# Kernel optimization log

Measured on AMD Instinct MI355X. Metric: run time of the kernel, lower is better.

The kernel has to match this reference:

```python
import jax, jax.numpy as jnp
import numpy as np

B, T, SEG = 64, 16, 50          # batch, n segments, segment length (cap 50 in original)
E, D, H, F = 512, 512, 8, 2048  # dim_embeddings, dim_encoder, n_heads, dim_ff
DH = D // H
SCALE = float(1.0 / np.sqrt(DH))


def _ln(x, g, b):
    m = jnp.mean(x, -1, keepdims=True)
    v = jnp.var(x, -1, keepdims=True)
    return (x - m) * jax.lax.rsqrt(v + 1e-5) * g + b


def _mha(q_in, kv_in, Wq, Wk, Wv, Wo, kv_lens):
    b, sq, _ = q_in.shape
    sk = kv_in.shape[1]
    q = (q_in @ Wq).reshape(b, sq, H, DH)
    k = (kv_in @ Wk).reshape(b, sk, H, DH)
    v = (kv_in @ Wv).reshape(b, sk, H, DH)
    scores = jnp.einsum('bqhd,bkhd->bhqk', q, k) * SCALE
    mask = jnp.arange(sk)[None, :] < kv_lens[:, None]  # [b, sk] key-padding mask
    scores = jnp.where(mask[:, None, None, :], scores, -1e9)
    a = jax.nn.softmax(scores, axis=-1)
    o = jnp.einsum('bhqk,bkhd->bqhd', a, v).reshape(b, sq, D)
    return o @ Wo


def _ffn(x, W1, W2):
    return jax.nn.relu(x @ W1) @ W2


def _encoder(x, lens, p):
    # TransformerEncoder: project E->D, masked self-attn + FFN, post-LN residuals
    h = x @ p['eWin']
    h = _ln(h + _mha(h, h, p['eWq'], p['eWk'], p['eWv'], p['eWo'], lens), p['eG1'], p['eB1'])
    return _ln(h + _ffn(h, p['eF1'], p['eF2']), p['eG2'], p['eB2'])


def _connection(prev, curr, prev_lens, p):
    # Connection: curr cross-attends over prev (masked by prev_lens) + FFN
    h = _ln(curr + _mha(curr, prev, p['cWq'], p['cWk'], p['cWv'], p['cWo'], prev_lens), p['cG1'], p['cB1'])
    return _ln(h + _ffn(h, p['cF1'], p['cF2']), p['cG2'], p['cB2'])


def _forward(seqs, ends, p):
    first_lens = jnp.minimum(ends[:, 0], SEG)
    encoded = _encoder(seqs[:, :SEG], first_lens, p)  # [B, SEG, D]
    # regular segmentation: ends[b,t] = (t+1)*SEG, so every step uses a full segment
    segs = seqs.reshape(B, T, SEG, E).transpose(1, 0, 2, 3)[1:]        # [T-1, B, SEG, E]
    seg_lens = jnp.minimum(ends[:, 1:] - ends[:, :-1], SEG).T          # [T-1, B]
    prev_lens = jnp.full((B,), SEG, jnp.int32)

    def step(enc, xs):
        seg, lens = xs
        currs = _encoder(seg, lens, p)
        out = _connection(enc, currs, prev_lens, p)
        return out, None  # out[-SEG:] == out since seq_len = min(diff, 50) = SEG

    encoded, _ = jax.lax.scan(step, encoded, (segs, seg_lens))
    return encoded


def setup_inputs():
    key = jax.random.key(0)
    ks = jax.random.split(key, 16)
    g = lambda k, s: jax.random.normal(k, s, jnp.float32) * 0.02
    inp = {
        'seqs': jax.random.normal(ks[0], (B, T * SEG, E), jnp.float32),
        'ends': jnp.broadcast_to((jnp.arange(1, T + 1) * SEG).astype(jnp.int32), (B, T)),
        'eWin': g(ks[1], (E, D)),
        'eWq': g(ks[2], (D, D)), 'eWk': g(ks[3], (D, D)),
        'eWv': g(ks[4], (D, D)), 'eWo': g(ks[5], (D, D)),
        'eG1': jnp.ones(D), 'eB1': jnp.zeros(D),
        'eF1': g(ks[6], (D, F)), 'eF2': g(ks[7], (F, D)),
        'eG2': jnp.ones(D), 'eB2': jnp.zeros(D),
        'cWq': g(ks[8], (D, D)), 'cWk': g(ks[9], (D, D)),
        'cWv': g(ks[10], (D, D)), 'cWo': g(ks[11], (D, D)),
        'cG1': jnp.ones(D), 'cB1': jnp.zeros(D),
        'cF1': g(ks[12], (D, F)), 'cF2': g(ks[13], (F, D)),
        'cG2': jnp.ones(D), 'cB2': jnp.zeros(D),
    }
    return inp


def reference(seqs, ends, eWin, eWq, eWk, eWv, eWo, eG1, eB1, eF1, eF2, eG2, eB2,
              cWq, cWk, cWv, cWo, cG1, cB1, cF1, cF2, cG2, cB2):
    p = dict(eWin=eWin, eWq=eWq, eWk=eWk, eWv=eWv, eWo=eWo, eG1=eG1, eB1=eB1,
             eF1=eF1, eF2=eF2, eG2=eG2, eB2=eB2, cWq=cWq, cWk=cWk, cWv=cWv,
             cWo=cWo, cG1=cG1, cB1=cB1, cF1=cF1, cF2=cF2, cG2=cG2, cB2=cB2)
    return _forward(seqs, ends, p)
```

## Files before the change

kernel.cpp:

```cpp
#include <hip/hip_runtime.h>


#define NB   64
#define NT   16
#define SEGL 50
#define DMODEL 512
#define DFF  2048
#define NHEAD 8
#define DHEAD 64

typedef unsigned short ushort_t;
typedef __attribute__((ext_vector_type(8))) short bfrag;
typedef __attribute__((ext_vector_type(4))) float ffrag;

__device__ __forceinline__ ushort_t f2b(float x) {
    union { float f; unsigned u; } c; c.f = x;
    unsigned r = c.u + 0x7fffu + ((c.u >> 16) & 1u);
    return (ushort_t)(r >> 16);
}

#define GLOAD_LDS16(g, l) __builtin_amdgcn_global_load_lds( \
    (const __attribute__((address_space(1))) void*)(g),      \
    (__attribute__((address_space(3))) void*)(l), 16, 0, 0)

template<int BM, int BN, int WROWS, int WCOLS>
__global__ __launch_bounds__(256) void mfma_gemm(
    const ushort_t* __restrict__ A, int agrp, long long astride,
    const ushort_t* __restrict__ Bt, ushort_t* __restrict__ C,
    int M, int N, int K, int relu)
{
    constexpr int WM = BM / WROWS, WN = BN / WCOLS;
    constexpr int SM = WM / 16, SN = WN / 16;
    constexpr int NSUBA = BM / 16, NSUBB = BN / 16;
    constexpr int NSUB = NSUBA + NSUBB;
    constexpr int NINST = NSUB * 2;
    constexpr int IPW = NINST / 4;
    constexpr int BUFS = NSUB * 1024;
    constexpr int EST = WN + 8;
    constexpr int LDS_KLOOP = 2 * BUFS;
    constexpr int LDS_EPI   = 4 * WM * EST;
    constexpr int LDS_SZ = LDS_KLOOP > LDS_EPI ? LDS_KLOOP : LDS_EPI;
    __shared__ ushort_t lds[LDS_SZ];

    const int tid = threadIdx.x;
    const int wave = tid >> 6, lane = tid & 63;
    const int wrow = wave / WCOLS, wcol = wave % WCOLS;
    const int bm = blockIdx.y * BM, bn = blockIdx.x * BN;
    const int lm = lane & 15, lq = lane >> 4;

    ffrag acc[SM][SN];
#pragma unroll
    for (int i = 0; i < SM; ++i)
#pragma unroll
        for (int j = 0; j < SN; ++j) acc[i][j] = (ffrag){0.f, 0.f, 0.f, 0.f};

    const ushort_t* gptr[IPW];
    int loff[IPW];
#pragma unroll
    for (int e = 0; e < IPW; ++e) {
        int g = wave * IPW + e;
        int s = g >> 1, h = g & 1;
        if (s < NSUBA) {
            int m = bm + s * 16 + lm;
            gptr[e] = A + (long long)(m / agrp) * astride
                        + (long long)(m % agrp) * K + h * 32 + lq * 8;
        } else {
            int n = bn + (s - NSUBA) * 16 + lm;
            gptr[e] = Bt + (long long)n * K + h * 32 + lq * 8;
        }
        loff[e] = s * 1024 + h * 512;
    }

#pragma unroll
    for (int e = 0; e < IPW; ++e)
        GLOAD_LDS16(gptr[e], &lds[loff[e]]);

    const int nk = K >> 6;
    for (int kk = 0; kk < nk; ++kk) {
        __syncthreads();
        if (kk + 1 < nk) {
            const int koff = (kk + 1) << 6;
            const int nb = (kk + 1) & 1;
#pragma unroll
            for (int e = 0; e < IPW; ++e)
                GLOAD_LDS16(gptr[e] + koff, &lds[nb * BUFS + loff[e]]);
        }
        const ushort_t* lb = &lds[(kk & 1) * BUFS];
#pragma unroll
        for (int h = 0; h < 2; ++h) {
            bfrag af[SM], bfg[SN];
#pragma unroll
            for (int i = 0; i < SM; ++i)
                af[i] = *(const bfrag*)&lb[(wrow * SM + i) * 1024 + h * 512 + lane * 8];
#pragma unroll
            for (int j = 0; j < SN; ++j)
                bfg[j] = *(const bfrag*)&lb[(NSUBA + wcol * SN + j) * 1024 + h * 512 + lane * 8];
#pragma unroll
            for (int i = 0; i < SM; ++i)
#pragma unroll
                for (int j = 0; j < SN; ++j)
                    acc[i][j] = __builtin_amdgcn_mfma_f32_16x16x32_bf16(
                        af[i], bfg[j], acc[i][j], 0, 0, 0);
        }
    }

    __syncthreads();
    ushort_t* ep = &lds[wave * WM * EST];
#pragma unroll
    for (int i = 0; i < SM; ++i)
#pragma unroll
        for (int j = 0; j < SN; ++j)
#pragma unroll
            for (int r = 0; r < 4; ++r) {
                int row = i * 16 + lq * 4 + r;
                int col = j * 16 + lm;
                float v = acc[i][j][r];
                if (relu) v = fmaxf(v, 0.f);
                ep[row * EST + col] = f2b(v);
            }
    constexpr int CPR = WN / 8;
    constexpr int RPI = 64 / CPR;
    const int lrow = lane / CPR, lcol = (lane % CPR) * 8;
#pragma unroll
    for (int it = 0; it < WM / RPI; ++it) {
        int row = it * RPI + lrow;
        uint4 v = *(const uint4*)&ep[row * EST + lcol];
        long long grow = bm + wrow * WM + row;
        int gcol = bn + wcol * WN + lcol;
        *(uint4*)&C[grow * N + gcol] = v;
    }
}

__global__ __launch_bounds__(256) void wtrans_k(
    const float* __restrict__ W, ushort_t* __restrict__ Wt, int K, int N)
{
    __shared__ float t[32][33];
    const int bk = blockIdx.y * 32, bn = blockIdx.x * 32;
    const int tx = threadIdx.x & 31, ty = threadIdx.x >> 5;
    for (int i = ty; i < 32; i += 8)
        t[i][tx] = W[(long long)(bk + i) * N + bn + tx];
    __syncthreads();
    for (int i = ty; i < 32; i += 8)
        Wt[(long long)(bn + i) * K + bk + tx] = f2b(t[tx][i]);
}

__global__ __launch_bounds__(256) void cvt_k(
    const float* __restrict__ in, ushort_t* __restrict__ out, long long n)
{
    long long i = ((long long)blockIdx.x * 256 + threadIdx.x) * 8;
    if (i >= n) return;
    float4 a = *(const float4*)(in + i);
    float4 b = *(const float4*)(in + i + 4);
    ushort_t o[8] = {f2b(a.x), f2b(a.y), f2b(a.z), f2b(a.w),
                     f2b(b.x), f2b(b.y), f2b(b.z), f2b(b.w)};
    *(uint4*)(out + i) = *(const uint4*)o;
}

__global__ __launch_bounds__(256) void attn_mfma_k(
    const ushort_t* __restrict__ Q, long long qns, long long qrs,
    const ushort_t* __restrict__ K, const ushort_t* __restrict__ V,
    long long kns, long long kvrs,
    ushort_t* __restrict__ O,
    const int* __restrict__ lens, int G, int t0)
{
    __shared__ ushort_t qs[64][72];
    __shared__ ushort_t ks[64][72];
    __shared__ ushort_t vt[64][72];
    const int n = blockIdx.x >> 3, h = blockIdx.x & 7;
    const int tid = threadIdx.x;
    const int wave = tid >> 6, lane = tid & 63;
    const int lm = lane & 15, lq = lane >> 4;
    int len = SEGL;
    if (lens) {
        int b = n / G, t = t0 + (n % G);
        len = lens[b * NT + t];
        if (len > SEGL) len = SEGL;
    }
    {
        uint4 z = {0, 0, 0, 0};
        uint4* vz = (uint4*)&vt[0][0];
        for (int i = tid; i < 64 * 72 / 8; i += 256) vz[i] = z;
    }
    __syncthreads();
    for (int idx = tid; idx < SEGL * 8; idx += 256) {
        int s = idx >> 3, d8 = (idx & 7) << 3;
        const ushort_t* qp = Q + (long long)n * qns + (long long)s * qrs + h * DHEAD + d8;
        const ushort_t* kp = K + (long long)n * kns + (long long)s * kvrs + h * DHEAD + d8;
        const ushort_t* vp = V + (long long)n * kns + (long long)s * kvrs + h * DHEAD + d8;
        *(uint4*)&qs[s][d8] = *(const uint4*)qp;
        *(uint4*)&ks[s][d8] = *(const uint4*)kp;
        uint4 v4 = *(const uint4*)vp;
        const ushort_t* vv = (const ushort_t*)&v4;
#pragma unroll
        for (int u = 0; u < 8; ++u) vt[d8 + u][s] = vv[u];
    }
    __syncthreads();

    ffrag sc[4];
#pragma unroll
    for (int nt = 0; nt < 4; ++nt) sc[nt] = (ffrag){0.f, 0.f, 0.f, 0.f};
#pragma unroll
    for (int kt = 0; kt < 2; ++kt) {
        bfrag a = *(const bfrag*)&qs[wave * 16 + lm][kt * 32 + lq * 8];
#pragma unroll
        for (int nt = 0; nt < 4; ++nt) {
            bfrag b = *(const bfrag*)&ks[nt * 16 + lm][kt * 32 + lq * 8];
            sc[nt] = __builtin_amdgcn_mfma_f32_16x16x32_bf16(a, b, sc[nt], 0, 0, 0);
        }
    }
    __syncthreads();

#pragma unroll
    for (int r = 0; r < 4; ++r) {
        float x[4];
        float mx = -1e30f;
#pragma unroll
        for (int nt = 0; nt < 4; ++nt) {
            int col = nt * 16 + lm;
            x[nt] = (col < len) ? sc[nt][r] * 0.125f : -1e9f;
            mx = fmaxf(mx, x[nt]);
        }
        for (int off = 8; off; off >>= 1) mx = fmaxf(mx, __shfl_xor(mx, off));
        float e[4], se = 0.f;
#pragma unroll
        for (int nt = 0; nt < 4; ++nt) { e[nt] = __expf(x[nt] - mx); se += e[nt]; }
        for (int off = 8; off; off >>= 1) se += __shfl_xor(se, off);
        float inv = 1.f / se;
        int row = wave * 16 + lq * 4 + r;
#pragma unroll
        for (int nt = 0; nt < 4; ++nt)
            qs[row][nt * 16 + lm] = f2b(e[nt] * inv);
    }
    __syncthreads();

    ffrag oc[4];
#pragma unroll
    for (int dt = 0; dt < 4; ++dt) oc[dt] = (ffrag){0.f, 0.f, 0.f, 0.f};
#pragma unroll
    for (int kt = 0; kt < 2; ++kt) {
        bfrag a = *(const bfrag*)&qs[wave * 16 + lm][kt * 32 + lq * 8];
#pragma unroll
        for (int dt = 0; dt < 4; ++dt) {
            bfrag b = *(const bfrag*)&vt[dt * 16 + lm][kt * 32 + lq * 8];
            oc[dt] = __builtin_amdgcn_mfma_f32_16x16x32_bf16(a, b, oc[dt], 0, 0, 0);
        }
    }
#pragma unroll
    for (int r = 0; r < 4; ++r) {
        int i = wave * 16 + lq * 4 + r;
        if (i < SEGL) {
            ushort_t* op = O + (long long)(n * SEGL + i) * DMODEL + h * DHEAD + lm;
#pragma unroll
            for (int dt = 0; dt < 4; ++dt)
                op[dt * 16] = f2b(oc[dt][r]);
        }
    }
}

__global__ __launch_bounds__(256) void cross_attn_k(
    const ushort_t* __restrict__ Qp, long long qns, long long qrs,
    const ushort_t* __restrict__ Prev, int pgrp, long long pstride,
    const ushort_t* __restrict__ Wkv,
    ushort_t* __restrict__ O)
{
    __shared__ ushort_t xp[64 * 264];
    __shared__ ushort_t qs[64][72];
    const int n = blockIdx.x >> 3, h = blockIdx.x & 7;
    const int tid = threadIdx.x;
    const int wave = tid >> 6, lane = tid & 63;
    const int lm = lane & 15, lq = lane >> 4;

    for (int idx = tid; idx < SEGL * 8; idx += 256) {
        int s = idx >> 3, d8 = (idx & 7) << 3;
        *(uint4*)&qs[s][d8] =
            *(const uint4*)(Qp + (long long)n * qns + (long long)s * qrs + h * DHEAD + d8);
    }

    const ushort_t* wbase = Wkv +
        (long long)((wave >> 1) * 512 + h * 64 + (wave & 1) * 32) * 512;
    ffrag kv[4][2];
#pragma unroll
    for (int i = 0; i < 4; ++i)
#pragma unroll
        for (int j = 0; j < 2; ++j) kv[i][j] = (ffrag){0.f, 0.f, 0.f, 0.f};

#pragma unroll
    for (int half = 0; half < 2; ++half) {
        __syncthreads();
        for (int idx = tid; idx < 64 * 33; idx += 256) {
            int s = idx / 33, c8 = (idx % 33) * 8;
            uint4 v = {0, 0, 0, 0};
            if (s < SEGL && c8 < 256) {
                long long r = (long long)n * SEGL + s;
                v = *(const uint4*)(Prev + (r / pgrp) * pstride
                                    + (r % pgrp) * DMODEL + half * 256 + c8);
            }
            *(uint4*)&xp[s * 264 + c8] = v;
        }
        __syncthreads();
#pragma unroll
        for (int k8 = 0; k8 < 8; ++k8) {
            const int kg = half * 256 + k8 * 32;
            bfrag bf[2], af[4];
#pragma unroll
            for (int j = 0; j < 2; ++j)
                bf[j] = *(const bfrag*)(wbase + (long long)(j * 16 + lm) * 512 + kg + lq * 8);
#pragma unroll
            for (int i = 0; i < 4; ++i)
                af[i] = *(const bfrag*)&xp[(i * 16 + lm) * 264 + k8 * 32 + lq * 8];
#pragma unroll
            for (int i = 0; i < 4; ++i)
#pragma unroll
                for (int j = 0; j < 2; ++j)
                    kv[i][j] = __builtin_amdgcn_mfma_f32_16x16x32_bf16(
                        af[i], bf[j], kv[i][j], 0, 0, 0);
        }
    }
    __syncthreads();
    ushort_t (*ks)[72] = (ushort_t(*)[72])&xp[0];
    ushort_t (*vt)[72] = (ushort_t(*)[72])&xp[64 * 72];
#pragma unroll
    for (int i = 0; i < 4; ++i)
#pragma unroll
        for (int j = 0; j < 2; ++j)
#pragma unroll
            for (int r = 0; r < 4; ++r) {
                int rowk = i * 16 + lq * 4 + r;
                int d = (wave & 1) * 32 + j * 16 + lm;
                ushort_t val = f2b(kv[i][j][r]);
                if (wave < 2) ks[rowk][d] = val;
                else          vt[d][rowk] = val;
            }
    __syncthreads();

    ffrag sc[4];
#pragma unroll
    for (int nt = 0; nt < 4; ++nt) sc[nt] = (ffrag){0.f, 0.f, 0.f, 0.f};
#pragma unroll
    for (int kt = 0; kt < 2; ++kt) {
        bfrag a = *(const bfrag*)&qs[wave * 16 + lm][kt * 32 + lq * 8];
#pragma unroll
        for (int nt = 0; nt < 4; ++nt) {
            bfrag b = *(const bfrag*)&ks[nt * 16 + lm][kt * 32 + lq * 8];
            sc[nt] = __builtin_amdgcn_mfma_f32_16x16x32_bf16(a, b, sc[nt], 0, 0, 0);
        }
    }
    __syncthreads();

#pragma unroll
    for (int r = 0; r < 4; ++r) {
        float x[4];
        float mx = -1e30f;
#pragma unroll
        for (int nt = 0; nt < 4; ++nt) {
            int col = nt * 16 + lm;
            x[nt] = (col < SEGL) ? sc[nt][r] * 0.125f : -1e9f;
            mx = fmaxf(mx, x[nt]);
        }
        for (int off = 8; off; off >>= 1) mx = fmaxf(mx, __shfl_xor(mx, off));
        float e[4], se = 0.f;
#pragma unroll
        for (int nt = 0; nt < 4; ++nt) { e[nt] = __expf(x[nt] - mx); se += e[nt]; }
        for (int off = 8; off; off >>= 1) se += __shfl_xor(se, off);
        float inv = 1.f / se;
        int row = wave * 16 + lq * 4 + r;
#pragma unroll
        for (int nt = 0; nt < 4; ++nt)
            qs[row][nt * 16 + lm] = f2b(e[nt] * inv);
    }
    __syncthreads();

    ffrag oc[4];
#pragma unroll
    for (int dt = 0; dt < 4; ++dt) oc[dt] = (ffrag){0.f, 0.f, 0.f, 0.f};
#pragma unroll
    for (int kt = 0; kt < 2; ++kt) {
        bfrag a = *(const bfrag*)&qs[wave * 16 + lm][kt * 32 + lq * 8];
#pragma unroll
        for (int dt = 0; dt < 4; ++dt) {
            bfrag b = *(const bfrag*)&vt[dt * 16 + lm][kt * 32 + lq * 8];
            oc[dt] = __builtin_amdgcn_mfma_f32_16x16x32_bf16(a, b, oc[dt], 0, 0, 0);
        }
    }
#pragma unroll
    for (int r = 0; r < 4; ++r) {
        int i = wave * 16 + lq * 4 + r;
        if (i < SEGL) {
            ushort_t* op = O + (long long)(n * SEGL + i) * DMODEL + h * DHEAD + lm;
#pragma unroll
            for (int dt = 0; dt < 4; ++dt)
                op[dt * 16] = f2b(oc[dt][r]);
        }
    }
}

template<bool OUTF32>
__global__ __launch_bounds__(256) void add_ln_k(
    const ushort_t* __restrict__ A, int agrp, long long astride,
    const ushort_t* __restrict__ Bv,
    const float* __restrict__ gamma, const float* __restrict__ beta,
    void* __restrict__ O, int ogrp, long long ostride, int M)
{
    const int wave = threadIdx.x >> 6, lane = threadIdx.x & 63;
    const int r = blockIdx.x * 4 + wave;
    if (r >= M) return;
    const ushort_t* a = A + (long long)(r / agrp) * astride + (long long)(r % agrp) * DMODEL;
    const ushort_t* b = Bv + (long long)r * DMODEL;
    float x[8];
    {
        uint4 a4 = *(const uint4*)(a + lane * 8);
        uint4 b4 = *(const uint4*)(b + lane * 8);
        const unsigned* aa = (const unsigned*)&a4;
        const unsigned* bb = (const unsigned*)&b4;
#pragma unroll
        for (int c = 0; c < 4; ++c) {
            union { unsigned u; float f; } alo, ahi, blo, bhi;
            alo.u = aa[c] << 16; ahi.u = aa[c] & 0xffff0000u;
            blo.u = bb[c] << 16; bhi.u = bb[c] & 0xffff0000u;
            x[2 * c]     = alo.f + blo.f;
            x[2 * c + 1] = ahi.f + bhi.f;
        }
    }
    float s = 0.f, s2 = 0.f;
#pragma unroll
    for (int i = 0; i < 8; ++i) { s += x[i]; s2 = fmaf(x[i], x[i], s2); }
    for (int off = 32; off; off >>= 1) {
        s += __shfl_xor(s, off);
        s2 += __shfl_xor(s2, off);
    }
    const float mean = s * (1.f / DMODEL);
    const float var = s2 * (1.f / DMODEL) - mean * mean;
    const float inv = rsqrtf(var + 1e-5f);
    float4 g0 = *(const float4*)(gamma + lane * 8);
    float4 g1 = *(const float4*)(gamma + lane * 8 + 4);
    float4 be0 = *(const float4*)(beta + lane * 8);
    float4 be1 = *(const float4*)(beta + lane * 8 + 4);
    float y[8];
    y[0] = (x[0] - mean) * inv * g0.x + be0.x;
    y[1] = (x[1] - mean) * inv * g0.y + be0.y;
    y[2] = (x[2] - mean) * inv * g0.z + be0.z;
    y[3] = (x[3] - mean) * inv * g0.w + be0.w;
    y[4] = (x[4] - mean) * inv * g1.x + be1.x;
    y[5] = (x[5] - mean) * inv * g1.y + be1.y;
    y[6] = (x[6] - mean) * inv * g1.z + be1.z;
    y[7] = (x[7] - mean) * inv * g1.w + be1.w;
    if (OUTF32) {
        float* o = (float*)O + (long long)(r / ogrp) * ostride + (long long)(r % ogrp) * DMODEL;
        *(float4*)(o + lane * 8) = *(float4*)&y[0];
        *(float4*)(o + lane * 8 + 4) = *(float4*)&y[4];
    } else {
        ushort_t* o = (ushort_t*)O + (long long)(r / ogrp) * ostride + (long long)(r % ogrp) * DMODEL;
        ushort_t ob[8];
#pragma unroll
        for (int i = 0; i < 8; ++i) ob[i] = f2b(y[i]);
        *(uint4*)(o + lane * 8) = *(const uint4*)ob;
    }
}

__global__ void lens_k(const int* __restrict__ ends, int* __restrict__ lens)
{
    int i = blockIdx.x * 256 + threadIdx.x;
    if (i >= NB * NT) return;
    int t = i & (NT - 1);
    int prev = t ? ends[i - 1] : 0;
    int l = ends[i] - prev;
    if (l > SEGL) l = SEGL;
    lens[i] = l;
}

extern "C" void kernel_launch(void* const* d_in, const int* in_sizes, int n_in,
                              void* d_out, int out_size, void* d_ws, size_t ws_size,
                              hipStream_t stream)
{
    const float* seqs = (const float*)d_in[0];
    const int*   ends = (const int*)d_in[1];
    const float* eG1 = (const float*)d_in[7],  *eB1 = (const float*)d_in[8];
    const float* eG2 = (const float*)d_in[11], *eB2 = (const float*)d_in[12];
    const float* cG1 = (const float*)d_in[17], *cB1 = (const float*)d_in[18];
    const float* cG2 = (const float*)d_in[21], *cB2 = (const float*)d_in[22];
    float* out = (float*)d_out;

    const int G = (ws_size >= (size_t)470000000) ? 8 : 4;
    const long long CH = 1638400LL * G;

    ushort_t* ws = (ushort_t*)d_ws;
    const long long SEQROW = (long long)NT * SEGL * DMODEL;
    ushort_t* SEQB = ws;
    ushort_t* WT   = SEQB + 26214400LL;
    ushort_t* ENC  = WT   + 6553600LL;
    ushort_t* BUF0 = ENC  + 26214400LL;
    ushort_t* QKV  = BUF0 + CH;
    ushort_t* BUF4 = QKV  + 3 * CH;
    ushort_t* BUF1 = BUF4 + CH;
    ushort_t* BUF2 = BUF1 + CH;
    ushort_t* MID  = BUF2 + CH;
    ushort_t* OUTB = MID  + 4 * CH;
    ushort_t* QALL = OUTB + 1638400LL;
    int*      lens = (int*)(QALL + 24576000LL);

    const ushort_t* eWinT = WT + 0;
    const ushort_t* WQKVe = WT + 262144;
    const ushort_t* eWoT  = WT + 1048576;
    const ushort_t* eF1T  = WT + 1310720;
    const ushort_t* eF2T  = WT + 2359296;
    const ushort_t* cWqT  = WT + 3407872;
    const ushort_t* cKV   = WT + 3670016;
    const ushort_t* cWoT  = WT + 4194304;
    const ushort_t* cF1T  = WT + 4456448;
    const ushort_t* cF2T  = WT + 5505024;

    struct WMap { int src; long long dst; int K, N; };
    const WMap wm[13] = {
        {2,  0,       512, 512},
        {3,  262144,  512, 512},
        {4,  524288,  512, 512},
        {5,  786432,  512, 512},
        {6,  1048576, 512, 512},
        {9,  1310720, 512, 2048},
        {10, 2359296, 2048, 512},
        {13, 3407872, 512, 512},
        {14, 3670016, 512, 512},
        {15, 3932160, 512, 512},
        {16, 4194304, 512, 512},
        {19, 4456448, 512, 2048},
        {20, 5505024, 2048, 512},
    };

    cvt_k<<<12800, 256, 0, stream>>>(seqs, SEQB, 26214400LL);
    for (int w = 0; w < 13; ++w) {
        dim3 g(wm[w].N / 32, wm[w].K / 32);
        wtrans_k<<<g, 256, 0, stream>>>((const float*)d_in[wm[w].src],
                                        WT + wm[w].dst, wm[w].K, wm[w].N);
    }
    lens_k<<<4, 256, 0, stream>>>(ends, lens);

    auto gemmL = [&](const ushort_t* A, int agrp, long long astr, const ushort_t* Bt,
                     ushort_t* C, int M, int N, int K, int relu) {
        dim3 g(N / 128, M / 128);
        mfma_gemm<128, 128, 2, 2><<<g, 256, 0, stream>>>(A, agrp, astr, Bt, C, M, N, K, relu);
    };
    auto gemmS = [&](const ushort_t* A, int agrp, long long astr, const ushort_t* Bt,
                     ushort_t* C, int M, int N, int K, int relu) {
        dim3 g(N / 64, M / 64);
        mfma_gemm<64, 64, 2, 2><<<g, 256, 0, stream>>>(A, agrp, astr, Bt, C, M, N, K, relu);
    };

    const int Mc = NB * G * SEGL;
    for (int c = 0; c < NT / G; ++c) {
        const int t0 = c * G;
        const ushort_t* Abase = SEQB + (long long)t0 * SEGL * DMODEL;
        ushort_t* ENCc = ENC + (long long)t0 * SEGL * DMODEL;
        gemmL(Abase, G * SEGL, SEQROW, eWinT, BUF0, Mc, 512, 512, 0);
        gemmL(BUF0, Mc, 0, WQKVe, QKV, Mc, 1536, 512, 0);
        attn_mfma_k<<<NB * G * NHEAD, 256, 0, stream>>>(
            QKV, 50LL * 1536, 1536, QKV + 512, QKV + 1024, 50LL * 1536, 1536,
            BUF4, lens, G, t0);
        gemmL(BUF4, Mc, 0, eWoT, BUF1, Mc, 512, 512, 0);
        add_ln_k<false><<<Mc / 4, 256, 0, stream>>>(BUF0, Mc, 0, BUF1, eG1, eB1,
                                                    BUF2, Mc, 0, Mc);
        gemmL(BUF2, Mc, 0, eF1T, MID, Mc, 2048, 512, 1);
        gemmL(MID, Mc, 0, eF2T, BUF1, Mc, 512, 2048, 0);
        add_ln_k<false><<<Mc / 4, 256, 0, stream>>>(BUF2, Mc, 0, BUF1, eG2, eB2,
                                                    ENCc, G * SEGL, SEQROW, Mc);
    }

    gemmL(ENC + 25600, 750, SEQROW, cWqT, QALL, 48000, 512, 512, 0);

    const int Ms = NB * SEGL;
    for (int t = 1; t < NT; ++t) {
        const ushort_t* currA = ENC + (long long)t * SEGL * DMODEL;
        const ushort_t* prevA; int pg; long long ps;
        if (t == 1) { prevA = ENC;  pg = SEGL; ps = SEQROW; }
        else        { prevA = OUTB; pg = Ms;   ps = 0; }
        cross_attn_k<<<NB * NHEAD, 256, 0, stream>>>(
            QALL + (long long)(t - 1) * 25600, 750LL * 512, 512,
            prevA, pg, ps, cKV, BUF4);
        gemmS(BUF4, Ms, 0, cWoT, BUF0, Ms, 512, 512, 0);
        add_ln_k<false><<<Ms / 4, 256, 0, stream>>>(currA, SEGL, SEQROW, BUF0, cG1, cB1,
                                                    BUF2, Ms, 0, Ms);
        gemmS(BUF2, Ms, 0, cF1T, MID, Ms, 2048, 512, 1);
        gemmS(MID, Ms, 0, cF2T, BUF0, Ms, 512, 2048, 0);
        if (t == NT - 1)
            add_ln_k<true><<<Ms / 4, 256, 0, stream>>>(BUF2, Ms, 0, BUF0, cG2, cB2,
                                                       out, Ms, 0, Ms);
        else
            add_ln_k<false><<<Ms / 4, 256, 0, stream>>>(BUF2, Ms, 0, BUF0, cG2, cB2,
                                                        OUTB, Ms, 0, Ms);
    }
}
```

Measured before the change: 2.770 ms.

## Fuse sequential connection-stage loop into one persistent kernel with grid barriers

Replaces the 15-step host loop of six launches per step (cross-attention, Wo GEMM, add+LN, two FFN GEMMs, add+LN) with one persistent kernel. Work items are grid-strided and the phases are separated by an atomic-counter grid barrier that lens_k resets. The goal is to remove about 90 kernel launches and their inter-kernel gaps on the serial critical path. The risks are barrier spin cost, a deadlock-avoidance timeout that could silently break correctness, and the assumption that every block is co-resident (grid of 256 or 512 chosen from occupancy).

```diff
diff --git a/kernel.cpp b/kernel.cpp
--- a/kernel.cpp
+++ b/kernel.cpp
@@ -218,143 +218,6 @@
         for (int nt = 0; nt < 4; ++nt) {
             int col = nt * 16 + lm;
             x[nt] = (col < len) ? sc[nt][r] * 0.125f : -1e9f;
-            mx = fmaxf(mx, x[nt]);
-        }
-        for (int off = 8; off; off >>= 1) mx = fmaxf(mx, __shfl_xor(mx, off));
-        float e[4], se = 0.f;
-#pragma unroll
-        for (int nt = 0; nt < 4; ++nt) { e[nt] = __expf(x[nt] - mx); se += e[nt]; }
-        for (int off = 8; off; off >>= 1) se += __shfl_xor(se, off);
-        float inv = 1.f / se;
-        int row = wave * 16 + lq * 4 + r;
-#pragma unroll
-        for (int nt = 0; nt < 4; ++nt)
-            qs[row][nt * 16 + lm] = f2b(e[nt] * inv);
-    }
-    __syncthreads();
-
-    ffrag oc[4];
-#pragma unroll
-    for (int dt = 0; dt < 4; ++dt) oc[dt] = (ffrag){0.f, 0.f, 0.f, 0.f};
-#pragma unroll
-    for (int kt = 0; kt < 2; ++kt) {
-        bfrag a = *(const bfrag*)&qs[wave * 16 + lm][kt * 32 + lq * 8];
-#pragma unroll
-        for (int dt = 0; dt < 4; ++dt) {
-            bfrag b = *(const bfrag*)&vt[dt * 16 + lm][kt * 32 + lq * 8];
-            oc[dt] = __builtin_amdgcn_mfma_f32_16x16x32_bf16(a, b, oc[dt], 0, 0, 0);
-        }
-    }
-#pragma unroll
-    for (int r = 0; r < 4; ++r) {
-        int i = wave * 16 + lq * 4 + r;
-        if (i < SEGL) {
-            ushort_t* op = O + (long long)(n * SEGL + i) * DMODEL + h * DHEAD + lm;
-#pragma unroll
-            for (int dt = 0; dt < 4; ++dt)
-                op[dt * 16] = f2b(oc[dt][r]);
-        }
-    }
-}
-
-__global__ __launch_bounds__(256) void cross_attn_k(
-    const ushort_t* __restrict__ Qp, long long qns, long long qrs,
-    const ushort_t* __restrict__ Prev, int pgrp, long long pstride,
-    const ushort_t* __restrict__ Wkv,
-    ushort_t* __restrict__ O)
-{
-    __shared__ ushort_t xp[64 * 264];
-    __shared__ ushort_t qs[64][72];
-    const int n = blockIdx.x >> 3, h = blockIdx.x & 7;
-    const int tid = threadIdx.x;
-    const int wave = tid >> 6, lane = tid & 63;
-    const int lm = lane & 15, lq = lane >> 4;
-
-    for (int idx = tid; idx < SEGL * 8; idx += 256) {
-        int s = idx >> 3, d8 = (idx & 7) << 3;
-        *(uint4*)&qs[s][d8] =
-            *(const uint4*)(Qp + (long long)n * qns + (long long)s * qrs + h * DHEAD + d8);
-    }
-
-    const ushort_t* wbase = Wkv +
-        (long long)((wave >> 1) * 512 + h * 64 + (wave & 1) * 32) * 512;
-    ffrag kv[4][2];
-#pragma unroll
-    for (int i = 0; i < 4; ++i)
-#pragma unroll
-        for (int j = 0; j < 2; ++j) kv[i][j] = (ffrag){0.f, 0.f, 0.f, 0.f};
-
-#pragma unroll
-    for (int half = 0; half < 2; ++half) {
-        __syncthreads();
-        for (int idx = tid; idx < 64 * 33; idx += 256) {
-            int s = idx / 33, c8 = (idx % 33) * 8;
-            uint4 v = {0, 0, 0, 0};
-            if (s < SEGL && c8 < 256) {
-                long long r = (long long)n * SEGL + s;
-                v = *(const uint4*)(Prev + (r / pgrp) * pstride
-                                    + (r % pgrp) * DMODEL + half * 256 + c8);
-            }
-            *(uint4*)&xp[s * 264 + c8] = v;
-        }
-        __syncthreads();
-#pragma unroll
-        for (int k8 = 0; k8 < 8; ++k8) {
-            const int kg = half * 256 + k8 * 32;
-            bfrag bf[2], af[4];
-#pragma unroll
-            for (int j = 0; j < 2; ++j)
-                bf[j] = *(const bfrag*)(wbase + (long long)(j * 16 + lm) * 512 + kg + lq * 8);
-#pragma unroll
-            for (int i = 0; i < 4; ++i)
-                af[i] = *(const bfrag*)&xp[(i * 16 + lm) * 264 + k8 * 32 + lq * 8];
-#pragma unroll
-            for (int i = 0; i < 4; ++i)
-#pragma unroll
-                for (int j = 0; j < 2; ++j)
-                    kv[i][j] = __builtin_amdgcn_mfma_f32_16x16x32_bf16(
-                        af[i], bf[j], kv[i][j], 0, 0, 0);
-        }
-    }
-    __syncthreads();
-    ushort_t (*ks)[72] = (ushort_t(*)[72])&xp[0];
-    ushort_t (*vt)[72] = (ushort_t(*)[72])&xp[64 * 72];
-#pragma unroll
-    for (int i = 0; i < 4; ++i)
-#pragma unroll
-        for (int j = 0; j < 2; ++j)
-#pragma unroll
-            for (int r = 0; r < 4; ++r) {
-                int rowk = i * 16 + lq * 4 + r;
-                int d = (wave & 1) * 32 + j * 16 + lm;
-                ushort_t val = f2b(kv[i][j][r]);
-                if (wave < 2) ks[rowk][d] = val;
-                else          vt[d][rowk] = val;
-            }
-    __syncthreads();
-
-    ffrag sc[4];
-#pragma unroll
-    for (int nt = 0; nt < 4; ++nt) sc[nt] = (ffrag){0.f, 0.f, 0.f, 0.f};
-#pragma unroll
-    for (int kt = 0; kt < 2; ++kt) {
-        bfrag a = *(const bfrag*)&qs[wave * 16 + lm][kt * 32 + lq * 8];
-#pragma unroll
-        for (int nt = 0; nt < 4; ++nt) {
-            bfrag b = *(const bfrag*)&ks[nt * 16 + lm][kt * 32 + lq * 8];
-            sc[nt] = __builtin_amdgcn_mfma_f32_16x16x32_bf16(a, b, sc[nt], 0, 0, 0);
-        }
-    }
-    __syncthreads();
-
-#pragma unroll
-    for (int r = 0; r < 4; ++r) {
-        float x[4];
-        float mx = -1e30f;
-#pragma unroll
-        for (int nt = 0; nt < 4; ++nt) {
-            int col = nt * 16 + lm;
-            x[nt] = (col < SEGL) ? sc[nt][r] * 0.125f : -1e9f;
             mx = fmaxf(mx, x[nt]);
         }
         for (int off = 8; off; off >>= 1) mx = fmaxf(mx, __shfl_xor(mx, off));
@@ -457,15 +320,389 @@
     }
 }
 
-__global__ void lens_k(const int* __restrict__ ends, int* __restrict__ lens)
+__global__ void lens_k(const int* __restrict__ ends, int* __restrict__ lens,
+                       unsigned* __restrict__ bar)
 {
     int i = blockIdx.x * 256 + threadIdx.x;
+    if (blockIdx.x == 0 && threadIdx.x == 0) *bar = 0;
     if (i >= NB * NT) return;
     int t = i & (NT - 1);
     int prev = t ? ends[i - 1] : 0;
     int l = ends[i] - prev;
     if (l > SEGL) l = SEGL;
     lens[i] = l;
+}
+
+
+__device__ __forceinline__ void gbar(unsigned* bar, unsigned target)
+{
+    __syncthreads();
+    if (threadIdx.x == 0) {
+        __threadfence();
+        __hip_atomic_fetch_add(bar, 1u, __ATOMIC_RELAXED, __HIP_MEMORY_SCOPE_AGENT);
+        int spins = 0;
+        while (__hip_atomic_load(bar, __ATOMIC_RELAXED, __HIP_MEMORY_SCOPE_AGENT) < target) {
+            __builtin_amdgcn_s_sleep(8);
+            if (++spins > (1 << 20)) break;
+        }
+        __threadfence();
+    }
+    __syncthreads();
+}
+
+__device__ void dev_gemm64(ushort_t* lds, int u,
+    const ushort_t* __restrict__ A, int agrp, long long astride,
+    const ushort_t* __restrict__ Bt, ushort_t* __restrict__ C,
+    int M, int N, int K, int relu)
+{
+    const int tid = threadIdx.x;
+    const int wave = tid >> 6, lane = tid & 63;
+    const int wrow = wave >> 1, wcol = wave & 1;
+    const int nbx = N >> 6;
+    const int bm = (u / nbx) << 6, bn = (u % nbx) << 6;
+    const int lm = lane & 15, lq = lane >> 4;
+
+    __syncthreads();
+
+    ffrag acc[2][2];
+#pragma unroll
+    for (int i = 0; i < 2; ++i)
+#pragma unroll
+        for (int j = 0; j < 2; ++j) acc[i][j] = (ffrag){0.f, 0.f, 0.f, 0.f};
+
+    const ushort_t* gptr[4];
+    int loff[4];
+#pragma unroll
+    for (int e = 0; e < 4; ++e) {
+        int g = wave * 4 + e;
+        int s = g >> 1, h = g & 1;
+        if (s < 4) {
+            int m = bm + s * 16 + lm;
+            gptr[e] = A + (long long)(m / agrp) * astride
+                        + (long long)(m % agrp) * K + h * 32 + lq * 8;
+        } else {
+            int n = bn + (s - 4) * 16 + lm;
+            gptr[e] = Bt + (long long)n * K + h * 32 + lq * 8;
+        }
+        loff[e] = s * 1024 + h * 512;
+    }
+
+#pragma unroll
+    for (int e = 0; e < 4; ++e)
+        GLOAD_LDS16(gptr[e], &lds[loff[e]]);
+
+    const int nk = K >> 6;
+    for (int kk = 0; kk < nk; ++kk) {
+        __syncthreads();
+        if (kk + 1 < nk) {
+            const int koff = (kk + 1) << 6;
+            const int nb = (kk + 1) & 1;
+#pragma unroll
+            for (int e = 0; e < 4; ++e)
+                GLOAD_LDS16(gptr[e] + koff, &lds[nb * 8192 + loff[e]]);
+        }
+        const ushort_t* lb = &lds[(kk & 1) * 8192];
+#pragma unroll
+        for (int h = 0; h < 2; ++h) {
+            bfrag af[2], bfg[2];
+#pragma unroll
+            for (int i = 0; i < 2; ++i)
+                af[i] = *(const bfrag*)&lb[(wrow * 2 + i) * 1024 + h * 512 + lane * 8];
+#pragma unroll
+            for (int j = 0; j < 2; ++j)
+                bfg[j] = *(const bfrag*)&lb[(4 + wcol * 2 + j) * 1024 + h * 512 + lane * 8];
+#pragma unroll
+            for (int i = 0; i < 2; ++i)
+#pragma unroll
+                for (int j = 0; j < 2; ++j)
+                    acc[i][j] = __builtin_amdgcn_mfma_f32_16x16x32_bf16(
+                        af[i], bfg[j], acc[i][j], 0, 0, 0);
+        }
+    }
+
+    __syncthreads();
+    ushort_t* ep = &lds[wave * 32 * 40];
+#pragma unroll
+    for (int i = 0; i < 2; ++i)
+#pragma unroll
+        for (int j = 0; j < 2; ++j)
+#pragma unroll
+            for (int r = 0; r < 4; ++r) {
+                int row = i * 16 + lq * 4 + r;
+                int col = j * 16 + lm;
+                float v = acc[i][j][r];
+                if (relu) v = fmaxf(v, 0.f);
+                ep[row * 40 + col] = f2b(v);
+            }
+    const int lrow = lane >> 2, lcol = (lane & 3) * 8;
+#pragma unroll
+    for (int it = 0; it < 2; ++it) {
+        int row = it * 16 + lrow;
+        uint4 v = *(const uint4*)&ep[row * 40 + lcol];
+        long long grow = bm + wrow * 32 + row;
+        int gcol = bn + wcol * 32 + lcol;
+        *(uint4*)&C[grow * N + gcol] = v;
+    }
+}
+
+__device__ void dev_cross_attn(ushort_t* smem, int u,
+    const ushort_t* __restrict__ Qp, long long qns, long long qrs,
+    const ushort_t* __restrict__ Prev, int pgrp, long long pstride,
+    const ushort_t* __restrict__ Wkv, ushort_t* __restrict__ O)
+{
+    ushort_t* xp = smem;
+    ushort_t (*qs)[72] = (ushort_t (*)[72])(smem + 64 * 264);
+    const int n = u >> 3, h = u & 7;
+    const int tid = threadIdx.x;
+    const int wave = tid >> 6, lane = tid & 63;
+    const int lm = lane & 15, lq = lane >> 4;
+
+    __syncthreads();
+
+    for (int idx = tid; idx < SEGL * 8; idx += 256) {
+        int s = idx >> 3, d8 = (idx & 7) << 3;
+        *(uint4*)&qs[s][d8] =
+            *(const uint4*)(Qp + (long long)n * qns + (long long)s * qrs + h * DHEAD + d8);
+    }
+
+    const ushort_t* wbase = Wkv +
+        (long long)((wave >> 1) * 512 + h * 64 + (wave & 1) * 32) * 512;
+    ffrag kv[4][2];
+#pragma unroll
+    for (int i = 0; i < 4; ++i)
+#pragma unroll
+        for (int j = 0; j < 2; ++j) kv[i][j] = (ffrag){0.f, 0.f, 0.f, 0.f};
+
+#pragma unroll
+    for (int half = 0; half < 2; ++half) {
+        __syncthreads();
+        for (int idx = tid; idx < 64 * 33; idx += 256) {
+            int s = idx / 33, c8 = (idx % 33) * 8;
+            uint4 v = {0, 0, 0, 0};
+            if (s < SEGL && c8 < 256) {
+                long long r = (long long)n * SEGL + s;
+                v = *(const uint4*)(Prev + (r / pgrp) * pstride
+                                    + (r % pgrp) * DMODEL + half * 256 + c8);
+            }
+            *(uint4*)&xp[s * 264 + c8] = v;
+        }
+        __syncthreads();
+#pragma unroll
+        for (int k8 = 0; k8 < 8; ++k8) {
+            const int kg = half * 256 + k8 * 32;
+            bfrag bf[2], af[4];
+#pragma unroll
+            for (int j = 0; j < 2; ++j)
+                bf[j] = *(const bfrag*)(wbase + (long long)(j * 16 + lm) * 512 + kg + lq * 8);
+#pragma unroll
+            for (int i = 0; i < 4; ++i)
+                af[i] = *(const bfrag*)&xp[(i * 16 + lm) * 264 + k8 * 32 + lq * 8];
+#pragma unroll
+            for (int i = 0; i < 4; ++i)
+#pragma unroll
+                for (int j = 0; j < 2; ++j)
+                    kv[i][j] = __builtin_amdgcn_mfma_f32_16x16x32_bf16(
+                        af[i], bf[j], kv[i][j], 0, 0, 0);
+        }
+    }
+    __syncthreads();
+    ushort_t (*ks)[72] = (ushort_t(*)[72])&xp[0];
+    ushort_t (*vt)[72] = (ushort_t(*)[72])&xp[64 * 72];
+#pragma unroll
+    for (int i = 0; i < 4; ++i)
+#pragma unroll
+        for (int j = 0; j < 2; ++j)
+#pragma unroll
+            for (int r = 0; r < 4; ++r) {
+                int rowk = i * 16 + lq * 4 + r;
+                int d = (wave & 1) * 32 + j * 16 + lm;
+                ushort_t val = f2b(kv[i][j][r]);
+                if (wave < 2) ks[rowk][d] = val;
+                else          vt[d][rowk] = val;
+            }
+    __syncthreads();
+
+    ffrag sc[4];
+#pragma unroll
+    for (int nt = 0; nt < 4; ++nt) sc[nt] = (ffrag){0.f, 0.f, 0.f, 0.f};
+#pragma unroll
+    for (int kt = 0; kt < 2; ++kt) {
+        bfrag a = *(const bfrag*)&qs[wave * 16 + lm][kt * 32 + lq * 8];
+#pragma unroll
+        for (int nt = 0; nt < 4; ++nt) {
+            bfrag b = *(const bfrag*)&ks[nt * 16 + lm][kt * 32 + lq * 8];
+            sc[nt] = __builtin_amdgcn_mfma_f32_16x16x32_bf16(a, b, sc[nt], 0, 0, 0);
+        }
+    }
+    __syncthreads();
+
+#pragma unroll
+    for (int r = 0; r < 4; ++r) {
+        float x[4];
+        float mx = -1e30f;
+#pragma unroll
+        for (int nt = 0; nt < 4; ++nt) {
+            int col = nt * 16 + lm;
+            x[nt] = (col < SEGL) ? sc[nt][r] * 0.125f : -1e9f;
+            mx = fmaxf(mx, x[nt]);
+        }
+        for (int off = 8; off; off >>= 1) mx = fmaxf(mx, __shfl_xor(mx, off));
+        float e[4], se = 0.f;
+#pragma unroll
+        for (int nt = 0; nt < 4; ++nt) { e[nt] = __expf(x[nt] - mx); se += e[nt]; }
+        for (int off = 8; off; off >>= 1) se += __shfl_xor(se, off);
+        float inv = 1.f / se;
+        int row = wave * 16 + lq * 4 + r;
+#pragma unroll
+        for (int nt = 0; nt < 4; ++nt)
+            qs[row][nt * 16 + lm] = f2b(e[nt] * inv);
+    }
+    __syncthreads();
+
+    ffrag oc[4];
+#pragma unroll
+    for (int dt = 0; dt < 4; ++dt) oc[dt] = (ffrag){0.f, 0.f, 0.f, 0.f};
+#pragma unroll
+    for (int kt = 0; kt < 2; ++kt) {
+        bfrag a = *(const bfrag*)&qs[wave * 16 + lm][kt * 32 + lq * 8];
+#pragma unroll
+        for (int dt = 0; dt < 4; ++dt) {
+            bfrag b = *(const bfrag*)&vt[dt * 16 + lm][kt * 32 + lq * 8];
+            oc[dt] = __builtin_amdgcn_mfma_f32_16x16x32_bf16(a, b, oc[dt], 0, 0, 0);
+        }
+    }
+#pragma unroll
+    for (int r = 0; r < 4; ++r) {
+        int i = wave * 16 + lq * 4 + r;
+        if (i < SEGL) {
+            ushort_t* op = O + (long long)(n * SEGL + i) * DMODEL + h * DHEAD + lm;
+#pragma unroll
+            for (int dt = 0; dt < 4; ++dt)
+                op[dt * 16] = f2b(oc[dt][r]);
+        }
+    }
+}
+
+template<bool OUTF32>
+__device__ void dev_add_ln(int u,
+    const ushort_t* __restrict__ A, int agrp, long long astride,
+    const ushort_t* __restrict__ Bv,
+    const float* __restrict__ gamma, const float* __restrict__ beta,
+    void* __restrict__ O, int ogrp, long long ostride, int M)
+{
+    const int wave = threadIdx.x >> 6, lane = threadIdx.x & 63;
+    const int r = u * 4 + wave;
+    if (r >= M) return;
+    const ushort_t* a = A + (long long)(r / agrp) * astride + (long long)(r % agrp) * DMODEL;
+    const ushort_t* b = Bv + (long long)r * DMODEL;
+    float x[8];
+    {
+        uint4 a4 = *(const uint4*)(a + lane * 8);
+        uint4 b4 = *(const uint4*)(b + lane * 8);
+        const unsigned* aa = (const unsigned*)&a4;
+        const unsigned* bb = (const unsigned*)&b4;
+#pragma unroll
+        for (int c = 0; c < 4; ++c) {
+            union { unsigned u; float f; } alo, ahi, blo, bhi;
+            alo.u = aa[c] << 16; ahi.u = aa[c] & 0xffff0000u;
+            blo.u = bb[c] << 16; bhi.u = bb[c] & 0xffff0000u;
+            x[2 * c]     = alo.f + blo.f;
+            x[2 * c + 1] = ahi.f + bhi.f;
+        }
+    }
+    float s = 0.f, s2 = 0.f;
+#pragma unroll
+    for (int i = 0; i < 8; ++i) { s += x[i]; s2 = fmaf(x[i], x[i], s2); }
+    for (int off = 32; off; off >>= 1) {
+        s += __shfl_xor(s, off);
+        s2 += __shfl_xor(s2, off);
+    }
+    const float mean = s * (1.f / DMODEL);
+    const float var = s2 * (1.f / DMODEL) - mean * mean;
+    const float inv = rsqrtf(var + 1e-5f);
+    float4 g0 = *(const float4*)(gamma + lane * 8);
+    float4 g1 = *(const float4*)(gamma + lane * 8 + 4);
+    float4 be0 = *(const float4*)(beta + lane * 8);
+    float4 be1 = *(const float4*)(beta + lane * 8 + 4);
+    float y[8];
+    y[0] = (x[0] - mean) * inv * g0.x + be0.x;
+    y[1] = (x[1] - mean) * inv * g0.y + be0.y;
+    y[2] = (x[2] - mean) * inv * g0.z + be0.z;
+    y[3] = (x[3] - mean) * inv * g0.w + be0.w;
+    y[4] = (x[4] - mean) * inv * g1.x + be1.x;
+    y[5] = (x[5] - mean) * inv * g1.y + be1.y;
+    y[6] = (x[6] - mean) * inv * g1.z + be1.z;
+    y[7] = (x[7] - mean) * inv * g1.w + be1.w;
+    if (OUTF32) {
+        float* o = (float*)O + (long long)(r / ogrp) * ostride + (long long)(r % ogrp) * DMODEL;
+        *(float4*)(o + lane * 8) = *(float4*)&y[0];
+        *(float4*)(o + lane * 8 + 4) = *(float4*)&y[4];
+    } else {
+        ushort_t* o = (ushort_t*)O + (long long)(r / ogrp) * ostride + (long long)(r % ogrp) * DMODEL;
+        ushort_t ob[8];
+#pragma unroll
+        for (int i = 0; i < 8; ++i) ob[i] = f2b(y[i]);
+        *(uint4*)(o + lane * 8) = *(const uint4*)ob;
+    }
+}
+
+__global__ __launch_bounds__(256, 2) void phase2_k(
+    const ushort_t* __restrict__ ENC, const ushort_t* __restrict__ QALL,
+    const ushort_t* __restrict__ cKV, const ushort_t* __restrict__ cWoT,
+    const ushort_t* __restrict__ cF1T, const ushort_t* __restrict__ cF2T,
+    const float* __restrict__ cG1, const float* __restrict__ cB1,
+    const float* __restrict__ cG2, const float* __restrict__ cB2,
+    ushort_t* __restrict__ BUF4, ushort_t* __restrict__ BUF0,
+    ushort_t* __restrict__ BUF2, ushort_t* __restrict__ MID,
+    ushort_t* __restrict__ OUTB, float* __restrict__ out,
+    unsigned* __restrict__ bar)
+{
+    __shared__ ushort_t smem[21504];
+    const int nblk = gridDim.x;
+    const int Ms = NB * SEGL;
+    const long long SEQROW = (long long)NT * SEGL * DMODEL;
+    unsigned target = 0;
+
+    for (int t = 1; t < NT; ++t) {
+        const ushort_t* prevA; int pg; long long ps;
+        if (t == 1) { prevA = ENC;  pg = SEGL; ps = SEQROW; }
+        else        { prevA = OUTB; pg = Ms;   ps = 0; }
+        const ushort_t* currA = ENC + (long long)t * SEGL * DMODEL;
+
+        for (int u = blockIdx.x; u < NB * NHEAD; u += nblk)
+            dev_cross_attn(smem, u,
+                           QALL + (long long)(t - 1) * 25600, 750LL * 512, 512,
+                           prevA, pg, ps, cKV, BUF4);
+        target += nblk; gbar(bar, target);
+
+        for (int u = blockIdx.x; u < (512 / 64) * (Ms / 64); u += nblk)
+            dev_gemm64(smem, u, BUF4, Ms, 0, cWoT, BUF0, Ms, 512, 512, 0);
+        target += nblk; gbar(bar, target);
+
+        for (int u = blockIdx.x; u < Ms / 4; u += nblk)
+            dev_add_ln<false>(u, currA, SEGL, SEQROW, BUF0, cG1, cB1,
+                              BUF2, Ms, 0, Ms);
+        target += nblk; gbar(bar, target);
+
+        for (int u = blockIdx.x; u < (2048 / 64) * (Ms / 64); u += nblk)
+            dev_gemm64(smem, u, BUF2, Ms, 0, cF1T, MID, Ms, 2048, 512, 1);
+        target += nblk; gbar(bar, target);
+
+        for (int u = blockIdx.x; u < (512 / 64) * (Ms / 64); u += nblk)
+            dev_gemm64(smem, u, MID, Ms, 0, cF2T, BUF0, Ms, 512, 2048, 0);
+        target += nblk; gbar(bar, target);
+
+        if (t == NT - 1) {
+            for (int u = blockIdx.x; u < Ms / 4; u += nblk)
+                dev_add_ln<true>(u, BUF2, Ms, 0, BUF0, cG2, cB2,
+                                 out, Ms, 0, Ms);
+        } else {
+            for (int u = blockIdx.x; u < Ms / 4; u += nblk)
+                dev_add_ln<false>(u, BUF2, Ms, 0, BUF0, cG2, cB2,
+                                  OUTB, Ms, 0, Ms);
+        }
+        target += nblk; gbar(bar, target);
+    }
 }
 
 extern "C" void kernel_launch(void* const* d_in, const int* in_sizes, int n_in,
@@ -497,6 +734,7 @@
     ushort_t* OUTB = MID  + 4 * CH;
     ushort_t* QALL = OUTB + 1638400LL;
     int*      lens = (int*)(QALL + 24576000LL);
+    unsigned* bar  = (unsigned*)(lens + 1024);
 
     const ushort_t* eWinT = WT + 0;
     const ushort_t* WQKVe = WT + 262144;
@@ -532,17 +770,12 @@
         wtrans_k<<<g, 256, 0, stream>>>((const float*)d_in[wm[w].src],
                                         WT + wm[w].dst, wm[w].K, wm[w].N);
     }
-    lens_k<<<4, 256, 0, stream>>>(ends, lens);
+    lens_k<<<4, 256, 0, stream>>>(ends, lens, bar);
 
     auto gemmL = [&](const ushort_t* A, int agrp, long long astr, const ushort_t* Bt,
                      ushort_t* C, int M, int N, int K, int relu) {
         dim3 g(N / 128, M / 128);
         mfma_gemm<128, 128, 2, 2><<<g, 256, 0, stream>>>(A, agrp, astr, Bt, C, M, N, K, relu);
-    };
-    auto gemmS = [&](const ushort_t* A, int agrp, long long astr, const ushort_t* Bt,
-                     ushort_t* C, int M, int N, int K, int relu) {
-        dim3 g(N / 64, M / 64);
-        mfma_gemm<64, 64, 2, 2><<<g, 256, 0, stream>>>(A, agrp, astr, Bt, C, M, N, K, relu);
     };
 
     const int Mc = NB * G * SEGL;
@@ -566,25 +799,18 @@
 
     gemmL(ENC + 25600, 750, SEQROW, cWqT, QALL, 48000, 512, 512, 0);
 
-    const int Ms = NB * SEGL;
-    for (int t = 1; t < NT; ++t) {
-        const ushort_t* currA = ENC + (long long)t * SEGL * DMODEL;
-        const ushort_t* prevA; int pg; long long ps;
-        if (t == 1) { prevA = ENC;  pg = SEGL; ps = SEQROW; }
-        else        { prevA = OUTB; pg = Ms;   ps = 0; }
-        cross_attn_k<<<NB * NHEAD, 256, 0, stream>>>(
-            QALL + (long long)(t - 1) * 25600, 750LL * 512, 512,
-            prevA, pg, ps, cKV, BUF4);
-        gemmS(BUF4, Ms, 0, cWoT, BUF0, Ms, 512, 512, 0);
-        add_ln_k<false><<<Ms / 4, 256, 0, stream>>>(currA, SEGL, SEQROW, BUF0, cG1, cB1,
-                                                    BUF2, Ms, 0, Ms);
-        gemmS(BUF2, Ms, 0, cF1T, MID, Ms, 2048, 512, 1);
-        gemmS(MID, Ms, 0, cF2T, BUF0, Ms, 512, 2048, 0);
-        if (t == NT - 1)
-            add_ln_k<true><<<Ms / 4, 256, 0, stream>>>(BUF2, Ms, 0, BUF0, cG2, cB2,
-                                                       out, Ms, 0, Ms);
-        else
-            add_ln_k<false><<<Ms / 4, 256, 0, stream>>>(BUF2, Ms, 0, BUF0, cG2, cB2,
-                                                        OUTB, Ms, 0, Ms);
-    }
-}
+    {
+        static int grid = 0;
+        if (grid == 0) {
+            int occ = 0;
+            if (hipOccupancyMaxActiveBlocksPerMultiprocessor(
+                    &occ, phase2_k, 256, 0) != hipSuccess || occ < 1)
+                occ = 1;
+            grid = (occ >= 2) ? 512 : 256;
+        }
+        phase2_k<<<grid, 256, 0, stream>>>(
+            ENC, QALL, cKV, cWoT, cF1T, cF2T,
+            cG1, cB1, cG2, cB2,
+            BUF4, BUF0, BUF2, MID, OUTB, out, bar);
+    }
+}
```

After: 5.346 ms. 93.0% more time.
